# Kernel optimization log

Hardware: AMD Instinct MI355X
Metric: run time of the kernel (lower is better)

The kernel has to match this reference:

```python
import jax, jax.numpy as jnp
import numpy as np

N_NODE = 100000
H = 128          # hidden_size
N_INTEREST = 4
B = 4096         # batch
T = 50           # session length


def setup_inputs() -> dict:
    key = jax.random.key(0)
    ks = jax.random.split(key, 8)
    stdv = 1.0 / np.sqrt(H)
    u = lambda k, s: jax.random.uniform(k, s, jnp.float32, -stdv, stdv)
    return {
        "inputs": jax.random.randint(ks[0], (B, T), 0, N_NODE),
        "embedding": u(ks[1], (N_NODE, H)),            # nn.Embedding weight
        "w_interest": u(ks[2], (N_INTEREST, H)),       # Linear(H -> n_interest, bias=False)
        "w_ih": u(ks[3], (N_INTEREST, 3 * H, H)),      # per-interest GNN params
        "w_hh": u(ks[4], (N_INTEREST, 3 * H, H)),
        "b_ih": u(ks[5], (N_INTEREST, 3 * H)),
        "b_hh": u(ks[6], (N_INTEREST, 3 * H)),
        "h0": jax.random.normal(ks[7], (N_INTEREST, B, H), jnp.float32),  # torch.randn init state
    }


def _gru_interest(w_ih, w_hh, b_ih, b_hh, h0, g_t, x_t):
    """Custom gated recurrence for one interest. x_t: [T,B,H], g_t: [T,B]."""
    def step(h, inp):
        x, gv = inp
        gi = x @ w_ih.T + b_ih          # [B, 3H]
        gh = h @ w_hh.T + b_hh          # [B, 3H]
        i_r, i_i, i_n = jnp.split(gi, 3, axis=1)
        h_r, h_i, h_n = jnp.split(gh, 3, axis=1)
        resetgate = jax.nn.sigmoid(i_r + h_r)
        inputgate = jax.nn.sigmoid(i_i + h_i)
        newgate = jnp.tanh(i_n + resetgate * h_n)
        g = gv[:, None]                  # [B, 1]
        concentrgate = jnp.where(g > 0.01, 1.0, 0.0) * g * inputgate
        hy = (1.0 - concentrgate) * h + concentrgate * newgate
        return hy, None
    h_last, _ = jax.lax.scan(step, h0, (x_t, g_t))
    return h_last                        # [B, H]


def reference(inputs, embedding, w_interest, w_ih, w_hh, b_ih, b_hh, h0):
    hidden = embedding[inputs]                                   # [B, T, H]
    # item_weight_for_interest: softmax over interests with temperature 0.1
    g = jax.nn.softmax((hidden @ w_interest.T) / 0.1, axis=2)    # [B, T, I]
    x_t = jnp.transpose(hidden, (1, 0, 2))                       # [T, B, H]
    g_t = jnp.transpose(g, (2, 1, 0))                            # [I, T, B]
    out = jax.vmap(_gru_interest, in_axes=(0, 0, 0, 0, 0, 0, None))(
        w_ih, w_hh, b_ih, b_hh, h0, g_t, x_t)                    # [I, B, H]
    return jnp.transpose(out, (1, 0, 2))                         # [B, I, H]
```

## Files before the change

### kernel.cpp

```cpp
#include <hip/hip_runtime.h>
#include <hip/hip_bf16.h>

#define NB 4096
#define NT 50
#define NH 128
#define NINT 4
#define ROWS 64

typedef float f32x4 __attribute__((ext_vector_type(4)));
typedef __bf16 bf16x8 __attribute__((ext_vector_type(8)));
typedef short short8 __attribute__((ext_vector_type(8)));

#define L2E 1.4426950408889634f

__device__ __forceinline__ float frcp(float x) { return __builtin_amdgcn_rcpf(x); }

__device__ __forceinline__ float exp2neg(float x) {
  float r;
  asm("v_exp_f32 %0, -%1" : "=v"(r) : "v"(x));
  return r;
}

__device__ __forceinline__ unsigned short bfbits(float f) {
  __bf16 b = (__bf16)f;
  return __builtin_bit_cast(unsigned short, b);
}

__global__ __launch_bounds__(512, 2)
void gru_fused(const int* __restrict__ inputs, const float* __restrict__ emb,
               const float* __restrict__ w_int, const float* __restrict__ w_ih,
               const float* __restrict__ w_hh, const float* __restrict__ b_ih,
               const float* __restrict__ b_hh, const float* __restrict__ h0,
               float* __restrict__ out) {
  __shared__ unsigned short xs[2][ROWS * NH];
  __shared__ unsigned short hs[2][ROWS * NH];
  __shared__ __align__(16) float gall[NT * ROWS];
  __shared__ int idxs[NT * ROWS];

  const int tid = threadIdx.x;
  const int bx = blockIdx.x;
  const int I = bx >> 6;
  const int R0 = (bx & 63) * ROWS;
  const int w = tid >> 6;
  const int lane = tid & 63;
  const int l15 = lane & 15;
  const int l4 = lane >> 4;
  const int col = w * 16 + l15;

  const int sr = tid >> 3;
  const int sp = tid & 7;

  for (int e = tid; e < NT * ROWS; e += 512) {
    int t = e >> 6, r = e & (ROWS - 1);
    idxs[e] = inputs[(size_t)(R0 + r) * NT + t];
  }
  __syncthreads();

  {
    float4 wv[NINT][4];
    #pragma unroll
    for (int i = 0; i < NINT; ++i) {
      const float4* p = (const float4*)(w_int + i * NH + sp * 16);
      #pragma unroll
      for (int q = 0; q < 4; ++q) wv[i][q] = p[q];
    }
    for (int t = 0; t < NT; ++t) {
      int e = t * ROWS + sr;
      const float4* xr = (const float4*)(emb + (size_t)idxs[e] * NH + sp * 16);
      float4 a = xr[0], b = xr[1], c = xr[2], dd = xr[3];
      float d[NINT];
      #pragma unroll
      for (int i = 0; i < NINT; ++i) {
        d[i] = a.x * wv[i][0].x + a.y * wv[i][0].y + a.z * wv[i][0].z + a.w * wv[i][0].w +
               b.x * wv[i][1].x + b.y * wv[i][1].y + b.z * wv[i][1].z + b.w * wv[i][1].w +
               c.x * wv[i][2].x + c.y * wv[i][2].y + c.z * wv[i][2].z + c.w * wv[i][2].w +
               dd.x * wv[i][3].x + dd.y * wv[i][3].y + dd.z * wv[i][3].z + dd.w * wv[i][3].w;
      }
      #pragma unroll
      for (int off = 1; off < 8; off <<= 1) {
        #pragma unroll
        for (int i = 0; i < NINT; ++i) d[i] += __shfl_xor(d[i], off, 64);
      }
      if (sp == 0) {
        float sa = d[0] * 10.f, sb = d[1] * 10.f, sc = d[2] * 10.f, sd = d[3] * 10.f;
        float mx = fmaxf(fmaxf(sa, sb), fmaxf(sc, sd));
        float ea = __expf(sa - mx), eb = __expf(sb - mx), ec = __expf(sc - mx),
              ed = __expf(sd - mx);
        float sel = (I == 0) ? ea : (I == 1) ? eb : (I == 2) ? ec : ed;
        float gv = sel * frcp(ea + eb + ec + ed);
        gall[e] = (gv > 0.01f) ? gv : 0.0f;
      }
    }
  }

  bf16x8 wih[3][4], whh[3][4];
  float biasRI[2];
  float biasNI, biasNH;
  {
    const float gs[3] = {L2E, L2E, 2.0f * L2E};
    #pragma unroll
    for (int g = 0; g < 3; ++g) {
      int oc = g * NH + col;
      #pragma unroll
      for (int kk = 0; kk < 4; ++kk) {
        int k0 = kk * 32 + l4 * 8;
        const float* pi = w_ih + ((size_t)(I * 384 + oc) * NH + k0);
        const float* ph = w_hh + ((size_t)(I * 384 + oc) * NH + k0);
        bf16x8 si, sh;
        #pragma unroll
        for (int e = 0; e < 8; ++e) {
          si[e] = (__bf16)(pi[e] * gs[g]);
          sh[e] = (__bf16)(ph[e] * gs[g]);
        }
        wih[g][kk] = si;
        whh[g][kk] = sh;
      }
    }
    biasRI[0] = (b_ih[I * 384 + col] + b_hh[I * 384 + col]) * L2E;
    biasRI[1] = (b_ih[I * 384 + NH + col] + b_hh[I * 384 + NH + col]) * L2E;
    biasNI = b_ih[I * 384 + 2 * NH + col] * (2.0f * L2E);
    biasNH = b_hh[I * 384 + 2 * NH + col] * (2.0f * L2E);
  }

  float hm[4][4];
  #pragma unroll
  for (int m = 0; m < 4; ++m) {
    #pragma unroll
    for (int j = 0; j < 4; ++j) {
      int row = m * 16 + l4 * 4 + j;
      float v = h0[((size_t)I * NB + R0 + row) * NH + col];
      hm[m][j] = v;
      hs[0][(row * NH + col) ^ ((row & 7) << 3)] = bfbits(v);
    }
  }

  {
    const float4* src = (const float4*)(emb + (size_t)idxs[sr] * NH + sp * 16);
    float4 v0 = src[0], v1 = src[1], v2 = src[2], v3 = src[3];
    short8 s0, s1;
    s0[0] = bfbits(v0.x); s0[1] = bfbits(v0.y); s0[2] = bfbits(v0.z); s0[3] = bfbits(v0.w);
    s0[4] = bfbits(v1.x); s0[5] = bfbits(v1.y); s0[6] = bfbits(v1.z); s0[7] = bfbits(v1.w);
    s1[0] = bfbits(v2.x); s1[1] = bfbits(v2.y); s1[2] = bfbits(v2.z); s1[3] = bfbits(v2.w);
    s1[4] = bfbits(v3.x); s1[5] = bfbits(v3.y); s1[6] = bfbits(v3.z); s1[7] = bfbits(v3.w);
    int base = sr * NH + sp * 16;
    int sw = (sr & 7) << 3;
    *(short8*)&xs[0][base ^ sw] = s0;
    *(short8*)&xs[0][(base + 8) ^ sw] = s1;
  }
  __syncthreads();

  for (int t = 0; t < NT; ++t) {
    const int cur = t & 1, nxt = cur ^ 1;
    const bool pf = (t + 1 < NT);

    float4 v0, v1, v2, v3;
    if (pf) {
      const float4* src =
          (const float4*)(emb + (size_t)idxs[(t + 1) * ROWS + sr] * NH + sp * 16);
      v0 = src[0]; v1 = src[1]; v2 = src[2]; v3 = src[3];
    }

    const unsigned short* hsc = hs[cur];
    const unsigned short* xsc = xs[cur];
    unsigned short* hsn = hs[nxt];

    #pragma unroll
    for (int m = 0; m < 4; ++m) {
      f32x4 aR = f32x4{biasRI[0], biasRI[0], biasRI[0], biasRI[0]};
      f32x4 aI = f32x4{biasRI[1], biasRI[1], biasRI[1], biasRI[1]};
      f32x4 aNI = f32x4{biasNI, biasNI, biasNI, biasNI};
      f32x4 aNH = f32x4{biasNH, biasNH, biasNH, biasNH};

      int arow = m * 16 + l15;
      int alin = arow * NH + l4 * 8;
      int sw2 = (arow & 7) << 3;
      __builtin_amdgcn_s_setprio(1);
      #pragma unroll
      for (int kk = 0; kk < 4; ++kk) {
        int e = (alin + kk * 32) ^ sw2;
        bf16x8 ah = __builtin_bit_cast(bf16x8, *(const short8*)&hsc[e]);
        bf16x8 ax = __builtin_bit_cast(bf16x8, *(const short8*)&xsc[e]);
        aR = __builtin_amdgcn_mfma_f32_16x16x32_bf16(ax, wih[0][kk], aR, 0, 0, 0);
        aR = __builtin_amdgcn_mfma_f32_16x16x32_bf16(ah, whh[0][kk], aR, 0, 0, 0);
        aI = __builtin_amdgcn_mfma_f32_16x16x32_bf16(ax, wih[1][kk], aI, 0, 0, 0);
        aI = __builtin_amdgcn_mfma_f32_16x16x32_bf16(ah, whh[1][kk], aI, 0, 0, 0);
        aNI = __builtin_amdgcn_mfma_f32_16x16x32_bf16(ax, wih[2][kk], aNI, 0, 0, 0);
        aNH = __builtin_amdgcn_mfma_f32_16x16x32_bf16(ah, whh[2][kk], aNH, 0, 0, 0);
      }
      __builtin_amdgcn_s_setprio(0);

      const f32x4 gq = *(const f32x4*)&gall[t * ROWS + m * 16 + l4 * 4];
      #pragma unroll
      for (int j = 0; j < 4; ++j) {
        int row = m * 16 + l4 * 4 + j;
        float rg = frcp(1.0f + exp2neg(aR[j]));
        float ig = frcp(1.0f + exp2neg(aI[j]));
        float an = fmaf(rg, aNH[j], aNI[j]);
        float ng = fmaf(2.0f, frcp(1.0f + exp2neg(an)), -1.0f);
        float c = gq[j] * ig;
        float hy = fmaf(c, ng - hm[m][j], hm[m][j]);
        hm[m][j] = hy;
        hsn[(row * NH + col) ^ ((row & 7) << 3)] = bfbits(hy);
      }
    }

    if (pf) {
      short8 s0, s1;
      s0[0] = bfbits(v0.x); s0[1] = bfbits(v0.y); s0[2] = bfbits(v0.z); s0[3] = bfbits(v0.w);
      s0[4] = bfbits(v1.x); s0[5] = bfbits(v1.y); s0[6] = bfbits(v1.z); s0[7] = bfbits(v1.w);
      s1[0] = bfbits(v2.x); s1[1] = bfbits(v2.y); s1[2] = bfbits(v2.z); s1[3] = bfbits(v2.w);
      s1[4] = bfbits(v3.x); s1[5] = bfbits(v3.y); s1[6] = bfbits(v3.z); s1[7] = bfbits(v3.w);
      int base = sr * NH + sp * 16;
      int sw = (sr & 7) << 3;
      *(short8*)&xs[nxt][base ^ sw] = s0;
      *(short8*)&xs[nxt][(base + 8) ^ sw] = s1;
    }
    __syncthreads();
  }

  #pragma unroll
  for (int m = 0; m < 4; ++m) {
    #pragma unroll
    for (int j = 0; j < 4; ++j) {
      int row = m * 16 + l4 * 4 + j;
      out[(size_t)(R0 + row) * (NINT * NH) + I * NH + col] = hm[m][j];
    }
  }
}

extern "C" void kernel_launch(void* const* d_in, const int* in_sizes, int n_in,
                              void* d_out, int out_size, void* d_ws, size_t ws_size,
                              hipStream_t stream) {
  const int* inputs = (const int*)d_in[0];
  const float* emb = (const float*)d_in[1];
  const float* w_int = (const float*)d_in[2];
  const float* w_ih = (const float*)d_in[3];
  const float* w_hh = (const float*)d_in[4];
  const float* b_ih = (const float*)d_in[5];
  const float* b_hh = (const float*)d_in[6];
  const float* h0 = (const float*)d_in[7];
  float* out = (float*)d_out;

  dim3 grid(NINT * (NB / ROWS));
  dim3 block(512);
  gru_fused<<<grid, block, 0, stream>>>(inputs, emb, w_int, w_ih, w_hh, b_ih,
                                        b_hh, h0, out);
}
```

Before: 202.1 us.

## Fuse interest-gate softmax into per-step embedding prefetch, drop separate gate pass

The separate prologue pass, which gathered all 50 timesteps of embeddings to compute the softmax gates, is removed. Gates are now computed from the fp32 embedding values already prefetched for the next step and stored in a small double-buffered shared array. This saves a full second gather of the embedding rows and shrinks shared memory. In exchange it adds dot-product, shuffle and exp work to the recurrent loop's critical path, plus w_interest reads from LDS every step.

```diff
diff --git a/kernel.cpp b/kernel.cpp
--- a/kernel.cpp
+++ b/kernel.cpp
@@ -34,7 +34,8 @@
                float* __restrict__ out) {
   __shared__ unsigned short xs[2][ROWS * NH];
   __shared__ unsigned short hs[2][ROWS * NH];
-  __shared__ __align__(16) float gall[NT * ROWS];
+  __shared__ float gbuf[2][ROWS];
+  __shared__ float wintl[NINT * NH];
   __shared__ int idxs[NT * ROWS];
 
   const int tid = threadIdx.x;
@@ -54,44 +55,35 @@
     int t = e >> 6, r = e & (ROWS - 1);
     idxs[e] = inputs[(size_t)(R0 + r) * NT + t];
   }
+  wintl[tid] = w_int[tid];
   __syncthreads();
 
-  {
-    float4 wv[NINT][4];
+  auto gate_from = [&](int buf, float4 a, float4 b, float4 c, float4 e) {
+    float d[NINT];
     #pragma unroll
     for (int i = 0; i < NINT; ++i) {
-      const float4* p = (const float4*)(w_int + i * NH + sp * 16);
-      #pragma unroll
-      for (int q = 0; q < 4; ++q) wv[i][q] = p[q];
-    }
-    for (int t = 0; t < NT; ++t) {
-      int e = t * ROWS + sr;
-      const float4* xr = (const float4*)(emb + (size_t)idxs[e] * NH + sp * 16);
-      float4 a = xr[0], b = xr[1], c = xr[2], dd = xr[3];
-      float d[NINT];
-      #pragma unroll
-      for (int i = 0; i < NINT; ++i) {
-        d[i] = a.x * wv[i][0].x + a.y * wv[i][0].y + a.z * wv[i][0].z + a.w * wv[i][0].w +
-               b.x * wv[i][1].x + b.y * wv[i][1].y + b.z * wv[i][1].z + b.w * wv[i][1].w +
-               c.x * wv[i][2].x + c.y * wv[i][2].y + c.z * wv[i][2].z + c.w * wv[i][2].w +
-               dd.x * wv[i][3].x + dd.y * wv[i][3].y + dd.z * wv[i][3].z + dd.w * wv[i][3].w;
-      }
-      #pragma unroll
-      for (int off = 1; off < 8; off <<= 1) {
-        #pragma unroll
-        for (int i = 0; i < NINT; ++i) d[i] += __shfl_xor(d[i], off, 64);
-      }
-      if (sp == 0) {
-        float sa = d[0] * 10.f, sb = d[1] * 10.f, sc = d[2] * 10.f, sd = d[3] * 10.f;
-        float mx = fmaxf(fmaxf(sa, sb), fmaxf(sc, sd));
-        float ea = __expf(sa - mx), eb = __expf(sb - mx), ec = __expf(sc - mx),
-              ed = __expf(sd - mx);
-        float sel = (I == 0) ? ea : (I == 1) ? eb : (I == 2) ? ec : ed;
-        float gv = sel * frcp(ea + eb + ec + ed);
-        gall[e] = (gv > 0.01f) ? gv : 0.0f;
-      }
-    }
-  }
+      const float4* wq = (const float4*)&wintl[i * NH + sp * 16];
+      float4 w0 = wq[0], w1 = wq[1], w2 = wq[2], w3 = wq[3];
+      d[i] = a.x * w0.x + a.y * w0.y + a.z * w0.z + a.w * w0.w +
+             b.x * w1.x + b.y * w1.y + b.z * w1.z + b.w * w1.w +
+             c.x * w2.x + c.y * w2.y + c.z * w2.z + c.w * w2.w +
+             e.x * w3.x + e.y * w3.y + e.z * w3.z + e.w * w3.w;
+    }
+    #pragma unroll
+    for (int off = 1; off < 8; off <<= 1) {
+      #pragma unroll
+      for (int i = 0; i < NINT; ++i) d[i] += __shfl_xor(d[i], off, 64);
+    }
+    if (sp == 0) {
+      float sa = d[0] * 10.f, sb = d[1] * 10.f, sc = d[2] * 10.f, sd = d[3] * 10.f;
+      float mx = fmaxf(fmaxf(sa, sb), fmaxf(sc, sd));
+      float ea = __expf(sa - mx), eb = __expf(sb - mx), ec = __expf(sc - mx),
+            ed = __expf(sd - mx);
+      float sel = (I == 0) ? ea : (I == 1) ? eb : (I == 2) ? ec : ed;
+      float gv = sel * frcp(ea + eb + ec + ed);
+      gbuf[buf][sr] = (gv > 0.01f) ? gv : 0.0f;
+    }
+  };
 
   bf16x8 wih[3][4], whh[3][4];
   float biasRI[2];
@@ -146,6 +138,7 @@
     int sw = (sr & 7) << 3;
     *(short8*)&xs[0][base ^ sw] = s0;
     *(short8*)&xs[0][(base + 8) ^ sw] = s1;
+    gate_from(0, v0, v1, v2, v3);
   }
   __syncthreads();
 
@@ -189,7 +182,7 @@
       }
       __builtin_amdgcn_s_setprio(0);
 
-      const f32x4 gq = *(const f32x4*)&gall[t * ROWS + m * 16 + l4 * 4];
+      const f32x4 gq = *(const f32x4*)&gbuf[cur][m * 16 + l4 * 4];
       #pragma unroll
       for (int j = 0; j < 4; ++j) {
         int row = m * 16 + l4 * 4 + j;
@@ -214,6 +207,7 @@
       int sw = (sr & 7) << 3;
       *(short8*)&xs[nxt][base ^ sw] = s0;
       *(short8*)&xs[nxt][(base + 8) ^ sw] = s1;
+      gate_from(nxt, v0, v1, v2, v3);
     }
     __syncthreads();
   }
```

Result: faster. 195.7 us (-3.2%).

## Warp-specialize gather and gate computation into producer waves overlapping recurrence

Applied to the files above, without the earlier changes.

Adds four producer waves (768 threads per block) that gather embedding rows, compute the interest softmax gate per step, and stage both into double-buffered shared memory. The eight consumer waves run only the MFMA recurrence. This removes the up-front 50-step gate prepass and the per-step gather from the compute waves, so that work overlaps the recurrence. The full gate table shrinks to a two-slot buffer, cutting shared memory. In exchange, launch bounds rise to 768 threads at three blocks per CU, which tightens register limits and may cause spills given the large weight fragments held in registers. Barrier counts match between the two roles, but the block-wide sync now includes the producers.

```diff
diff --git a/kernel.cpp b/kernel.cpp
--- a/kernel.cpp
+++ b/kernel.cpp
@@ -26,7 +26,7 @@
   return __builtin_bit_cast(unsigned short, b);
 }
 
-__global__ __launch_bounds__(512, 2)
+__global__ __launch_bounds__(768, 3)
 void gru_fused(const int* __restrict__ inputs, const float* __restrict__ emb,
                const float* __restrict__ w_int, const float* __restrict__ w_ih,
                const float* __restrict__ w_hh, const float* __restrict__ b_ih,
@@ -34,7 +34,7 @@
                float* __restrict__ out) {
   __shared__ unsigned short xs[2][ROWS * NH];
   __shared__ unsigned short hs[2][ROWS * NH];
-  __shared__ __align__(16) float gall[NT * ROWS];
+  __shared__ __align__(16) float gbuf[2][ROWS];
   __shared__ int idxs[NT * ROWS];
 
   const int tid = threadIdx.x;
@@ -45,185 +45,183 @@
   const int lane = tid & 63;
   const int l15 = lane & 15;
   const int l4 = lane >> 4;
-  const int col = w * 16 + l15;
-
-  const int sr = tid >> 3;
-  const int sp = tid & 7;
-
-  for (int e = tid; e < NT * ROWS; e += 512) {
+
+  for (int e = tid; e < NT * ROWS; e += 768) {
     int t = e >> 6, r = e & (ROWS - 1);
     idxs[e] = inputs[(size_t)(R0 + r) * NT + t];
   }
   __syncthreads();
 
-  {
+  if (w < 8) {
+    const int col = w * 16 + l15;
+
+    bf16x8 wih[3][4], whh[3][4];
+    float biasRI[2], biasNI, biasNH;
+    {
+      const float gs[3] = {L2E, L2E, 2.0f * L2E};
+      #pragma unroll
+      for (int g = 0; g < 3; ++g) {
+        int oc = g * NH + col;
+        #pragma unroll
+        for (int kk = 0; kk < 4; ++kk) {
+          int k0 = kk * 32 + l4 * 8;
+          const float* pi = w_ih + ((size_t)(I * 384 + oc) * NH + k0);
+          const float* ph = w_hh + ((size_t)(I * 384 + oc) * NH + k0);
+          bf16x8 si, sh;
+          #pragma unroll
+          for (int e = 0; e < 8; ++e) {
+            si[e] = (__bf16)(pi[e] * gs[g]);
+            sh[e] = (__bf16)(ph[e] * gs[g]);
+          }
+          wih[g][kk] = si;
+          whh[g][kk] = sh;
+        }
+      }
+      biasRI[0] = (b_ih[I * 384 + col] + b_hh[I * 384 + col]) * L2E;
+      biasRI[1] = (b_ih[I * 384 + NH + col] + b_hh[I * 384 + NH + col]) * L2E;
+      biasNI = b_ih[I * 384 + 2 * NH + col] * (2.0f * L2E);
+      biasNH = b_hh[I * 384 + 2 * NH + col] * (2.0f * L2E);
+    }
+
+    float hm[4][4];
+    #pragma unroll
+    for (int m = 0; m < 4; ++m) {
+      #pragma unroll
+      for (int j = 0; j < 4; ++j) {
+        int row = m * 16 + l4 * 4 + j;
+        float v = h0[((size_t)I * NB + R0 + row) * NH + col];
+        hm[m][j] = v;
+        hs[0][(row * NH + col) ^ ((row & 7) << 3)] = bfbits(v);
+      }
+    }
+    __syncthreads();
+
+    for (int t = 0; t < NT; ++t) {
+      const int cur = t & 1, nxt = cur ^ 1;
+      const unsigned short* hsc = hs[cur];
+      const unsigned short* xsc = xs[cur];
+      unsigned short* hsn = hs[nxt];
+
+      #pragma unroll
+      for (int m = 0; m < 4; ++m) {
+        f32x4 aR = f32x4{biasRI[0], biasRI[0], biasRI[0], biasRI[0]};
+        f32x4 aI = f32x4{biasRI[1], biasRI[1], biasRI[1], biasRI[1]};
+        f32x4 aNI = f32x4{biasNI, biasNI, biasNI, biasNI};
+        f32x4 aNH = f32x4{biasNH, biasNH, biasNH, biasNH};
+
+        int arow = m * 16 + l15;
+        int alin = arow * NH + l4 * 8;
+        int sw2 = (arow & 7) << 3;
+        __builtin_amdgcn_s_setprio(1);
+        #pragma unroll
+        for (int kk = 0; kk < 4; ++kk) {
+          int e = (alin + kk * 32) ^ sw2;
+          bf16x8 ah = __builtin_bit_cast(bf16x8, *(const short8*)&hsc[e]);
+          bf16x8 ax = __builtin_bit_cast(bf16x8, *(const short8*)&xsc[e]);
+          aR = __builtin_amdgcn_mfma_f32_16x16x32_bf16(ax, wih[0][kk], aR, 0, 0, 0);
+          aR = __builtin_amdgcn_mfma_f32_16x16x32_bf16(ah, whh[0][kk], aR, 0, 0, 0);
+          aI = __builtin_amdgcn_mfma_f32_16x16x32_bf16(ax, wih[1][kk], aI, 0, 0, 0);
+          aI = __builtin_amdgcn_mfma_f32_16x16x32_bf16(ah, whh[1][kk], aI, 0, 0, 0);
+          aNI = __builtin_amdgcn_mfma_f32_16x16x32_bf16(ax, wih[2][kk], aNI, 0, 0, 0);
+          aNH = __builtin_amdgcn_mfma_f32_16x16x32_bf16(ah, whh[2][kk], aNH, 0, 0, 0);
+        }
+        __builtin_amdgcn_s_setprio(0);
+
+        const f32x4 gq = *(const f32x4*)&gbuf[cur][m * 16 + l4 * 4];
+        #pragma unroll
+        for (int j = 0; j < 4; ++j) {
+          int row = m * 16 + l4 * 4 + j;
+          float rg = frcp(1.0f + exp2neg(aR[j]));
+          float ig = frcp(1.0f + exp2neg(aI[j]));
+          float an = fmaf(rg, aNH[j], aNI[j]);
+          float ng = fmaf(2.0f, frcp(1.0f + exp2neg(an)), -1.0f);
+          float c = gq[j] * ig;
+          float hy = fmaf(c, ng - hm[m][j], hm[m][j]);
+          hm[m][j] = hy;
+          hsn[(row * NH + col) ^ ((row & 7) << 3)] = bfbits(hy);
+        }
+      }
+      __syncthreads();
+    }
+
+    #pragma unroll
+    for (int m = 0; m < 4; ++m) {
+      #pragma unroll
+      for (int j = 0; j < 4; ++j) {
+        int row = m * 16 + l4 * 4 + j;
+        out[(size_t)(R0 + row) * (NINT * NH) + I * NH + col] = hm[m][j];
+      }
+    }
+  } else {
+    const int stid = tid - 512;
+    const int gr = stid >> 3;
+    const int gp = stid & 7;
+
     float4 wv[NINT][4];
     #pragma unroll
     for (int i = 0; i < NINT; ++i) {
-      const float4* p = (const float4*)(w_int + i * NH + sp * 16);
+      const float4* p = (const float4*)(w_int + i * NH + gp * 16);
       #pragma unroll
       for (int q = 0; q < 4; ++q) wv[i][q] = p[q];
     }
-    for (int t = 0; t < NT; ++t) {
-      int e = t * ROWS + sr;
-      const float4* xr = (const float4*)(emb + (size_t)idxs[e] * NH + sp * 16);
-      float4 a = xr[0], b = xr[1], c = xr[2], dd = xr[3];
+
+    auto stage_row = [&](int buf, int r, float4 a, float4 b, float4 c, float4 e) {
       float d[NINT];
       #pragma unroll
       for (int i = 0; i < NINT; ++i) {
         d[i] = a.x * wv[i][0].x + a.y * wv[i][0].y + a.z * wv[i][0].z + a.w * wv[i][0].w +
                b.x * wv[i][1].x + b.y * wv[i][1].y + b.z * wv[i][1].z + b.w * wv[i][1].w +
                c.x * wv[i][2].x + c.y * wv[i][2].y + c.z * wv[i][2].z + c.w * wv[i][2].w +
-               dd.x * wv[i][3].x + dd.y * wv[i][3].y + dd.z * wv[i][3].z + dd.w * wv[i][3].w;
+               e.x * wv[i][3].x + e.y * wv[i][3].y + e.z * wv[i][3].z + e.w * wv[i][3].w;
       }
       #pragma unroll
       for (int off = 1; off < 8; off <<= 1) {
         #pragma unroll
         for (int i = 0; i < NINT; ++i) d[i] += __shfl_xor(d[i], off, 64);
       }
-      if (sp == 0) {
+      if (gp == 0) {
         float sa = d[0] * 10.f, sb = d[1] * 10.f, sc = d[2] * 10.f, sd = d[3] * 10.f;
         float mx = fmaxf(fmaxf(sa, sb), fmaxf(sc, sd));
         float ea = __expf(sa - mx), eb = __expf(sb - mx), ec = __expf(sc - mx),
               ed = __expf(sd - mx);
         float sel = (I == 0) ? ea : (I == 1) ? eb : (I == 2) ? ec : ed;
         float gv = sel * frcp(ea + eb + ec + ed);
-        gall[e] = (gv > 0.01f) ? gv : 0.0f;
-      }
-    }
-  }
-
-  bf16x8 wih[3][4], whh[3][4];
-  float biasRI[2];
-  float biasNI, biasNH;
-  {
-    const float gs[3] = {L2E, L2E, 2.0f * L2E};
-    #pragma unroll
-    for (int g = 0; g < 3; ++g) {
-      int oc = g * NH + col;
-      #pragma unroll
-      for (int kk = 0; kk < 4; ++kk) {
-        int k0 = kk * 32 + l4 * 8;
-        const float* pi = w_ih + ((size_t)(I * 384 + oc) * NH + k0);
-        const float* ph = w_hh + ((size_t)(I * 384 + oc) * NH + k0);
-        bf16x8 si, sh;
-        #pragma unroll
-        for (int e = 0; e < 8; ++e) {
-          si[e] = (__bf16)(pi[e] * gs[g]);
-          sh[e] = (__bf16)(ph[e] * gs[g]);
-        }
-        wih[g][kk] = si;
-        whh[g][kk] = sh;
-      }
-    }
-    biasRI[0] = (b_ih[I * 384 + col] + b_hh[I * 384 + col]) * L2E;
-    biasRI[1] = (b_ih[I * 384 + NH + col] + b_hh[I * 384 + NH + col]) * L2E;
-    biasNI = b_ih[I * 384 + 2 * NH + col] * (2.0f * L2E);
-    biasNH = b_hh[I * 384 + 2 * NH + col] * (2.0f * L2E);
-  }
-
-  float hm[4][4];
-  #pragma unroll
-  for (int m = 0; m < 4; ++m) {
-    #pragma unroll
-    for (int j = 0; j < 4; ++j) {
-      int row = m * 16 + l4 * 4 + j;
-      float v = h0[((size_t)I * NB + R0 + row) * NH + col];
-      hm[m][j] = v;
-      hs[0][(row * NH + col) ^ ((row & 7) << 3)] = bfbits(v);
-    }
-  }
-
-  {
-    const float4* src = (const float4*)(emb + (size_t)idxs[sr] * NH + sp * 16);
-    float4 v0 = src[0], v1 = src[1], v2 = src[2], v3 = src[3];
-    short8 s0, s1;
-    s0[0] = bfbits(v0.x); s0[1] = bfbits(v0.y); s0[2] = bfbits(v0.z); s0[3] = bfbits(v0.w);
-    s0[4] = bfbits(v1.x); s0[5] = bfbits(v1.y); s0[6] = bfbits(v1.z); s0[7] = bfbits(v1.w);
-    s1[0] = bfbits(v2.x); s1[1] = bfbits(v2.y); s1[2] = bfbits(v2.z); s1[3] = bfbits(v2.w);
-    s1[4] = bfbits(v3.x); s1[5] = bfbits(v3.y); s1[6] = bfbits(v3.z); s1[7] = bfbits(v3.w);
-    int base = sr * NH + sp * 16;
-    int sw = (sr & 7) << 3;
-    *(short8*)&xs[0][base ^ sw] = s0;
-    *(short8*)&xs[0][(base + 8) ^ sw] = s1;
-  }
-  __syncthreads();
-
-  for (int t = 0; t < NT; ++t) {
-    const int cur = t & 1, nxt = cur ^ 1;
-    const bool pf = (t + 1 < NT);
-
-    float4 v0, v1, v2, v3;
-    if (pf) {
-      const float4* src =
-          (const float4*)(emb + (size_t)idxs[(t + 1) * ROWS + sr] * NH + sp * 16);
-      v0 = src[0]; v1 = src[1]; v2 = src[2]; v3 = src[3];
-    }
-
-    const unsigned short* hsc = hs[cur];
-    const unsigned short* xsc = xs[cur];
-    unsigned short* hsn = hs[nxt];
-
-    #pragma unroll
-    for (int m = 0; m < 4; ++m) {
-      f32x4 aR = f32x4{biasRI[0], biasRI[0], biasRI[0], biasRI[0]};
-      f32x4 aI = f32x4{biasRI[1], biasRI[1], biasRI[1], biasRI[1]};
-      f32x4 aNI = f32x4{biasNI, biasNI, biasNI, biasNI};
-      f32x4 aNH = f32x4{biasNH, biasNH, biasNH, biasNH};
-
-      int arow = m * 16 + l15;
-      int alin = arow * NH + l4 * 8;
-      int sw2 = (arow & 7) << 3;
-      __builtin_amdgcn_s_setprio(1);
-      #pragma unroll
-      for (int kk = 0; kk < 4; ++kk) {
-        int e = (alin + kk * 32) ^ sw2;
-        bf16x8 ah = __builtin_bit_cast(bf16x8, *(const short8*)&hsc[e]);
-        bf16x8 ax = __builtin_bit_cast(bf16x8, *(const short8*)&xsc[e]);
-        aR = __builtin_amdgcn_mfma_f32_16x16x32_bf16(ax, wih[0][kk], aR, 0, 0, 0);
-        aR = __builtin_amdgcn_mfma_f32_16x16x32_bf16(ah, whh[0][kk], aR, 0, 0, 0);
-        aI = __builtin_amdgcn_mfma_f32_16x16x32_bf16(ax, wih[1][kk], aI, 0, 0, 0);
-        aI = __builtin_amdgcn_mfma_f32_16x16x32_bf16(ah, whh[1][kk], aI, 0, 0, 0);
-        aNI = __builtin_amdgcn_mfma_f32_16x16x32_bf16(ax, wih[2][kk], aNI, 0, 0, 0);
-        aNH = __builtin_amdgcn_mfma_f32_16x16x32_bf16(ah, whh[2][kk], aNH, 0, 0, 0);
-      }
-      __builtin_amdgcn_s_setprio(0);
-
-      const f32x4 gq = *(const f32x4*)&gall[t * ROWS + m * 16 + l4 * 4];
-      #pragma unroll
-      for (int j = 0; j < 4; ++j) {
-        int row = m * 16 + l4 * 4 + j;
-        float rg = frcp(1.0f + exp2neg(aR[j]));
-        float ig = frcp(1.0f + exp2neg(aI[j]));
-        float an = fmaf(rg, aNH[j], aNI[j]);
-        float ng = fmaf(2.0f, frcp(1.0f + exp2neg(an)), -1.0f);
-        float c = gq[j] * ig;
-        float hy = fmaf(c, ng - hm[m][j], hm[m][j]);
-        hm[m][j] = hy;
-        hsn[(row * NH + col) ^ ((row & 7) << 3)] = bfbits(hy);
-      }
-    }
-
-    if (pf) {
+        gbuf[buf][r] = (gv > 0.01f) ? gv : 0.0f;
+      }
       short8 s0, s1;
-      s0[0] = bfbits(v0.x); s0[1] = bfbits(v0.y); s0[2] = bfbits(v0.z); s0[3] = bfbits(v0.w);
-      s0[4] = bfbits(v1.x); s0[5] = bfbits(v1.y); s0[6] = bfbits(v1.z); s0[7] = bfbits(v1.w);
-      s1[0] = bfbits(v2.x); s1[1] = bfbits(v2.y); s1[2] = bfbits(v2.z); s1[3] = bfbits(v2.w);
-      s1[4] = bfbits(v3.x); s1[5] = bfbits(v3.y); s1[6] = bfbits(v3.z); s1[7] = bfbits(v3.w);
-      int base = sr * NH + sp * 16;
-      int sw = (sr & 7) << 3;
-      *(short8*)&xs[nxt][base ^ sw] = s0;
-      *(short8*)&xs[nxt][(base + 8) ^ sw] = s1;
+      s0[0] = bfbits(a.x); s0[1] = bfbits(a.y); s0[2] = bfbits(a.z); s0[3] = bfbits(a.w);
+      s0[4] = bfbits(b.x); s0[5] = bfbits(b.y); s0[6] = bfbits(b.z); s0[7] = bfbits(b.w);
+      s1[0] = bfbits(c.x); s1[1] = bfbits(c.y); s1[2] = bfbits(c.z); s1[3] = bfbits(c.w);
+      s1[4] = bfbits(e.x); s1[5] = bfbits(e.y); s1[6] = bfbits(e.z); s1[7] = bfbits(e.w);
+      int base = r * NH + gp * 16;
+      int sw = (r & 7) << 3;
+      *(short8*)&xs[buf][base ^ sw] = s0;
+      *(short8*)&xs[buf][(base + 8) ^ sw] = s1;
+    };
+
+    {
+      const float4* p0 = (const float4*)(emb + (size_t)idxs[gr] * NH + gp * 16);
+      const float4* p1 = (const float4*)(emb + (size_t)idxs[gr + 32] * NH + gp * 16);
+      float4 a0 = p0[0], b0 = p0[1], c0 = p0[2], d0 = p0[3];
+      float4 a1 = p1[0], b1 = p1[1], c1 = p1[2], d1 = p1[3];
+      stage_row(0, gr, a0, b0, c0, d0);
+      stage_row(0, gr + 32, a1, b1, c1, d1);
     }
     __syncthreads();
-  }
-
-  #pragma unroll
-  for (int m = 0; m < 4; ++m) {
-    #pragma unroll
-    for (int j = 0; j < 4; ++j) {
-      int row = m * 16 + l4 * 4 + j;
-      out[(size_t)(R0 + row) * (NINT * NH) + I * NH + col] = hm[m][j];
+
+    for (int t = 0; t < NT; ++t) {
+      const int nxt = (t & 1) ^ 1;
+      if (t + 1 < NT) {
+        const float4* p0 =
+            (const float4*)(emb + (size_t)idxs[(t + 1) * ROWS + gr] * NH + gp * 16);
+        const float4* p1 =
+            (const float4*)(emb + (size_t)idxs[(t + 1) * ROWS + gr + 32] * NH + gp * 16);
+        float4 a0 = p0[0], b0 = p0[1], c0 = p0[2], d0 = p0[3];
+        float4 a1 = p1[0], b1 = p1[1], c1 = p1[2], d1 = p1[3];
+        stage_row(nxt, gr, a0, b0, c0, d0);
+        stage_row(nxt, gr + 32, a1, b1, c1, d1);
+      }
+      __syncthreads();
     }
   }
 }
@@ -242,7 +240,7 @@
   float* out = (float*)d_out;
 
   dim3 grid(NINT * (NB / ROWS));
-  dim3 block(512);
+  dim3 block(768);
   gru_fused<<<grid, block, 0, stream>>>(inputs, emb, w_int, w_ih, w_hh, b_ih,
                                         b_hh, h0, out);
 }
```

Measured after the change: 222.5 us. 10.1% more time.
